# Kernel tuning notes

Hardware: AMD Instinct MI355X
Metric: run time of the kernel (lower is better)

## Reference

```python
import jax, jax.numpy as jnp
import numpy as np

N, E = 50000, 800000
IN, H, D, K = 256, 4, 64, 3
NEG_SLOPE = 0.2

def leaky_relu(x):
    return jnp.where(x >= 0, x, NEG_SLOPE * x)

def setup_inputs() -> dict:
    key = jax.random.key(0)
    ks = jax.random.split(key, 10)
    feat = jax.random.normal(ks[0], (N, IN), dtype=jnp.float32)
    src = jax.random.randint(ks[1], (E,), 0, N)
    dst = jax.random.randint(ks[2], (E,), 0, N)
    g = np.sqrt(2.0)  # relu gain used by xavier init; scale irrelevant to math
    W_src = jax.random.normal(ks[3], (H * D, IN), dtype=jnp.float32) * (g * np.sqrt(2.0 / (IN + H * D)))
    attn_l = jax.random.normal(ks[4], (1, H, D), dtype=jnp.float32) * 0.1
    attn_r = jax.random.normal(ks[5], (1, H, D), dtype=jnp.float32) * 0.1
    hop_attn_l = jax.random.normal(ks[6], (1, H, D), dtype=jnp.float32) * 0.1
    hop_attn_r = jax.random.normal(ks[7], (1, H, D), dtype=jnp.float32) * 0.1
    pos_emb = jax.random.normal(ks[8], (1, H, K + 1, D), dtype=jnp.float32) * 0.1
    bias = jnp.zeros((H * D,), dtype=jnp.float32)
    return {"feat": feat, "src": src, "dst": dst, "W_src": W_src,
            "attn_l": attn_l, "attn_r": attn_r, "hop_attn_l": hop_attn_l,
            "hop_attn_r": hop_attn_r, "pos_emb": pos_emb, "bias": bias}

def edge_softmax_dst(e, dst):
    # e: [E, H], softmax over incoming edges of each dst node
    m = jax.ops.segment_max(e, dst, num_segments=N)          # [N, H]
    m = jnp.where(jnp.isfinite(m), m, 0.0)                   # empty segments
    ex = jnp.exp(e - m[dst])                                 # [E, H]
    s = jax.ops.segment_sum(ex, dst, num_segments=N)         # [N, H]
    denom = s[dst]
    return jnp.where(denom > 0, ex / denom, 0.0)

def reference(feat, src, dst, W_src, attn_l, attn_r, hop_attn_l, hop_attn_r, pos_emb, bias):
    # fc_src (shared with fc_dst): [N, IN] -> [N, H, D]
    feat_src = (feat @ W_src.T).reshape(N, H, D)
    feat_dst = feat_src  # share_weights=True
    # GAT transition matrix, norm_by='dst'
    el = jnp.sum(feat_src * attn_l, axis=-1)   # [N, H]
    er = jnp.sum(feat_dst * attn_r, axis=-1)   # [N, H]
    e = leaky_relu(el[src] + er[dst])          # [E, H]
    a = edge_softmax_dst(e, dst)               # [E, H]
    # K-hop diffusion with positional embedding per hop
    h = feat_src
    hstack = [h + pos_emb[:, :, 0, :]]
    for k in range(1, K + 1):
        msg = a[:, :, None] * h[src]                          # [E, H, D]
        h = jax.ops.segment_sum(msg, dst, num_segments=N)     # [N, H, D]
        hstack.append(h + pos_emb[:, :, k, :])
    hs = jnp.stack(hstack, axis=2)                            # [N, H, K+1, D]
    # Hop-wise attention (HA)
    a_l = jnp.sum(hs * hop_attn_l[:, :, None, :], axis=-1, keepdims=True)            # [N,H,K+1,1]
    a_r = jnp.sum(hs[:, :, :1, :] * hop_attn_r[:, :, None, :], axis=-1, keepdims=True)  # [N,H,1,1]
    hop_a = jax.nn.softmax(leaky_relu(a_l + a_r), axis=2)
    rst = jnp.sum(hs * hop_a, axis=2)                         # [N, H, D]
    rst = rst + bias.reshape(1, H, D)
    return rst
```

## Files before the change

kernel.cpp:

```cpp
#include <hip/hip_runtime.h>
#include <hip/hip_bf16.h>
#include <hip/hip_fp16.h>

#define NN 50000
#define EE 800000
#define INF_ 256
#define HH 4
#define DD 64
#define KK 3
#define NEG_SLOPE 0.2f

struct __align__(8) half4 { __half2 a, b; };
struct __align__(8) short4s { short a, b, c, d; };

using bf16x8 = __attribute__((ext_vector_type(8))) short;
using f32x4  = __attribute__((ext_vector_type(4))) float;

__device__ __forceinline__ float lrelu(float x) {
    return x >= 0.0f ? x : NEG_SLOPE * x;
}

__device__ __forceinline__ float wave_sum(float v) {
    #pragma unroll
    for (int m = 1; m < 64; m <<= 1) v += __shfl_xor(v, m, 64);
    return v;
}

__device__ __forceinline__ short f2bf(float f) {
    union { float f; unsigned u; } v; v.f = f;
    unsigned r = (v.u + 0x7FFFu + ((v.u >> 16) & 1u)) >> 16;
    return (short)r;
}
__device__ __forceinline__ float bf2f(short s) {
    union { unsigned u; float f; } v; v.u = ((unsigned)(unsigned short)s) << 16;
    return v.f;
}

__global__ __launch_bounds__(256) void conv_w(const float* __restrict__ W,
                                              short* __restrict__ Wh,
                                              short* __restrict__ Wl) {
    int i = blockIdx.x * 256 + threadIdx.x;
    int e    = i & 7;
    int lane = (i >> 3) & 63;
    int tj   = (i >> 9) & 3;
    int kc   = (i >> 11) & 7;
    int w    = i >> 14;
    int j = w * 64 + tj * 16 + (lane & 15);
    int k = kc * 32 + (lane >> 4) * 8 + e;
    float v = W[j * 256 + k];
    short h = f2bf(v);
    Wh[i] = h;
    Wl[i] = f2bf(v - bf2f(h));
}

__global__ __launch_bounds__(256) void gemm_mfma(const float* __restrict__ A,
                                                 const short* __restrict__ Wh,
                                                 const short* __restrict__ Wl,
                                                 const float* __restrict__ al,
                                                 const float* __restrict__ ar,
                                                 float* __restrict__ C,
                                                 __half* __restrict__ C16,
                                                 float* __restrict__ el,
                                                 float* __restrict__ er, int M) {
    __shared__ short Ah[32 * 256];
    __shared__ short Al[32 * 256];
    int tid = threadIdx.x;
    int m0 = blockIdx.x * 32;

    {
        int r4 = tid >> 6;
        int c4 = (tid & 63) * 4;
        #pragma unroll
        for (int it = 0; it < 8; ++it) {
            int row = it * 4 + r4;
            int m = m0 + row;
            float4 v = (m < M) ? *(const float4*)&A[(size_t)m * 256 + c4]
                               : make_float4(0.f, 0.f, 0.f, 0.f);
            short h0 = f2bf(v.x), h1 = f2bf(v.y), h2 = f2bf(v.z), h3 = f2bf(v.w);
            short l0 = f2bf(v.x - bf2f(h0)), l1 = f2bf(v.y - bf2f(h1));
            short l2 = f2bf(v.z - bf2f(h2)), l3 = f2bf(v.w - bf2f(h3));
            int cs = c4 ^ ((row & 7) << 3);
            short4s sh = { h0, h1, h2, h3 };
            short4s sl = { l0, l1, l2, l3 };
            *(short4s*)&Ah[row * 256 + cs] = sh;
            *(short4s*)&Al[row * 256 + cs] = sl;
        }
    }
    __syncthreads();

    int w = tid >> 6;
    int lane = tid & 63;
    int lrow = lane & 15;
    int lk = lane >> 4;
    int j0 = w * 64;

    f32x4 acc[2][4] = {};

    #pragma unroll
    for (int kc = 0; kc < 8; ++kc) {
        int kbase = kc * 32 + lk * 8;
        int fbase = (((w * 8 + kc) * 4) * 64 + lane) * 8;
        bf16x8 bh[4], bl[4], ah[2], alo[2];
        #pragma unroll
        for (int tj = 0; tj < 4; ++tj) {
            bh[tj] = *(const bf16x8*)&Wh[fbase + tj * 64 * 8];
            bl[tj] = *(const bf16x8*)&Wl[fbase + tj * 64 * 8];
        }
        #pragma unroll
        for (int tm = 0; tm < 2; ++tm) {
            int row = tm * 16 + lrow;
            int ks = kbase ^ ((row & 7) << 3);
            ah[tm]  = *(const bf16x8*)&Ah[row * 256 + ks];
            alo[tm] = *(const bf16x8*)&Al[row * 256 + ks];
        }
        #pragma unroll
        for (int tm = 0; tm < 2; ++tm)
            #pragma unroll
            for (int tj = 0; tj < 4; ++tj) {
                acc[tm][tj] = __builtin_amdgcn_mfma_f32_16x16x32_bf16(ah[tm],  bh[tj], acc[tm][tj], 0, 0, 0);
                acc[tm][tj] = __builtin_amdgcn_mfma_f32_16x16x32_bf16(alo[tm], bh[tj], acc[tm][tj], 0, 0, 0);
                acc[tm][tj] = __builtin_amdgcn_mfma_f32_16x16x32_bf16(ah[tm],  bl[tj], acc[tm][tj], 0, 0, 0);
            }
    }

    #pragma unroll
    for (int tm = 0; tm < 2; ++tm)
        #pragma unroll
        for (int tj = 0; tj < 4; ++tj)
            #pragma unroll
            for (int r = 0; r < 4; ++r) {
                int m = m0 + tm * 16 + lk * 4 + r;
                if (m < M) {
                    int j = j0 + tj * 16 + lrow;
                    float x = acc[tm][tj][r];
                    C[(size_t)m * 256 + j] = x;
                    C16[(size_t)m * 256 + j] = __float2half(x);
                }
            }

    float alj[4], arj[4];
    #pragma unroll
    for (int tj = 0; tj < 4; ++tj) {
        alj[tj] = al[j0 + tj * 16 + lrow];
        arj[tj] = ar[j0 + tj * 16 + lrow];
    }
    #pragma unroll
    for (int tm = 0; tm < 2; ++tm)
        #pragma unroll
        for (int r = 0; r < 4; ++r) {
            float pl = acc[tm][0][r] * alj[0] + acc[tm][1][r] * alj[1] +
                       acc[tm][2][r] * alj[2] + acc[tm][3][r] * alj[3];
            float pr = acc[tm][0][r] * arj[0] + acc[tm][1][r] * arj[1] +
                       acc[tm][2][r] * arj[2] + acc[tm][3][r] * arj[3];
            #pragma unroll
            for (int msk = 1; msk < 16; msk <<= 1) {
                pl += __shfl_xor(pl, msk, 64);
                pr += __shfl_xor(pr, msk, 64);
            }
            if (lrow == 0) {
                int m = m0 + tm * 16 + lk * 4 + r;
                if (m < M) { el[m * 4 + w] = pl; er[m * 4 + w] = pr; }
            }
        }
}

__global__ void count_k(const int* __restrict__ dst, int* __restrict__ cnt, int E) {
    int e = blockIdx.x * 256 + threadIdx.x;
    if (e < E) atomicAdd(&cnt[dst[e]], 1);
}

__global__ __launch_bounds__(256) void scan1(const int* __restrict__ counts,
                                             int* __restrict__ offs,
                                             int* __restrict__ bsums, int n) {
    __shared__ int sh[256];
    int b = blockIdx.x, t = threadIdx.x;
    int base = b * 1024 + t * 4;
    int v[4];
    #pragma unroll
    for (int i = 0; i < 4; ++i) v[i] = (base + i < n) ? counts[base + i] : 0;
    int tsum = v[0] + v[1] + v[2] + v[3];
    sh[t] = tsum; __syncthreads();
    for (int off = 1; off < 256; off <<= 1) {
        int x = (t >= off) ? sh[t - off] : 0;
        __syncthreads();
        sh[t] += x;
        __syncthreads();
    }
    int run = sh[t] - tsum;
    #pragma unroll
    for (int i = 0; i < 4; ++i) { if (base + i < n) offs[base + i] = run; run += v[i]; }
    if (t == 255) bsums[b] = sh[255];
}

__global__ void scan2(int* bsums, int nb) {
    if (threadIdx.x == 0 && blockIdx.x == 0) {
        int run = 0;
        for (int i = 0; i < nb; ++i) { int v = bsums[i]; bsums[i] = run; run += v; }
    }
}

__global__ __launch_bounds__(256) void scan3(int* __restrict__ offs,
                                             const int* __restrict__ bsums,
                                             int* __restrict__ cursor, int n, int E) {
    int b = blockIdx.x;
    int base = b * 1024 + threadIdx.x * 4;
    int add = bsums[b];
    #pragma unroll
    for (int i = 0; i < 4; ++i) {
        if (base + i < n) {
            int v = offs[base + i] + add;
            offs[base + i] = v;
            cursor[base + i] = v;
        }
    }
    if (b == 0 && threadIdx.x == 0) offs[n] = E;
}

__global__ void scatter_edges(const int* __restrict__ src, const int* __restrict__ dst,
                              const float4* __restrict__ el4, const float4* __restrict__ er4,
                              int* __restrict__ cursor, int* __restrict__ ssrc,
                              float4* __restrict__ alog, int E) {
    int e = blockIdx.x * 256 + threadIdx.x;
    if (e >= E) return;
    int s = src[e], d = dst[e];
    int slot = atomicAdd(&cursor[d], 1);
    ssrc[slot] = s;
    float4 a = el4[s], b = er4[d];
    float4 o;
    o.x = lrelu(a.x + b.x);
    o.y = lrelu(a.y + b.y);
    o.z = lrelu(a.z + b.z);
    o.w = lrelu(a.w + b.w);
    alog[slot] = o;
}

__global__ __launch_bounds__(256) void edge_softmax(const int* __restrict__ offs,
                                                    float* __restrict__ alog, int n) {
    int t = blockIdx.x * 256 + threadIdx.x;
    if (t >= n * 4) return;
    int node = t >> 2, h = t & 3;
    int o0 = offs[node], o1 = offs[node + 1];
    if (o0 >= o1) return;
    float m = -1e30f;
    for (int i = o0; i < o1; ++i) m = fmaxf(m, alog[i * 4 + h]);
    float s = 0.f;
    for (int i = o0; i < o1; ++i) {
        float v = expf(alog[i * 4 + h] - m);
        alog[i * 4 + h] = v;
        s += v;
    }
    float inv = 1.0f / s;
    for (int i = o0; i < o1; ++i) alog[i * 4 + h] *= inv;
}

__global__ __launch_bounds__(256) void hop_kernel(const int* __restrict__ offs,
                                                  const int* __restrict__ ssrc,
                                                  const float* __restrict__ alog,
                                                  const __half* __restrict__ hin,
                                                  __half* __restrict__ hout) {
    int w = threadIdx.x >> 6;
    int n = blockIdx.x * 4 + w;
    if (n >= NN) return;
    int lane = threadIdx.x & 63;
    int h = lane >> 4;
    int col = lane * 4;
    int o0 = offs[n], o1 = offs[n + 1];
    float4 acc0 = make_float4(0.f, 0.f, 0.f, 0.f);
    float4 acc1 = make_float4(0.f, 0.f, 0.f, 0.f);
    float4 acc2 = make_float4(0.f, 0.f, 0.f, 0.f);
    float4 acc3 = make_float4(0.f, 0.f, 0.f, 0.f);
    int i = o0;
    for (; i + 4 <= o1; i += 4) {
        int s0 = ssrc[i], s1 = ssrc[i + 1], s2 = ssrc[i + 2], s3 = ssrc[i + 3];
        float a0 = alog[i * 4 + h];
        float a1 = alog[(i + 1) * 4 + h];
        float a2 = alog[(i + 2) * 4 + h];
        float a3 = alog[(i + 3) * 4 + h];
        half4 v0 = *(const half4*)&hin[(size_t)s0 * 256 + col];
        half4 v1 = *(const half4*)&hin[(size_t)s1 * 256 + col];
        half4 v2 = *(const half4*)&hin[(size_t)s2 * 256 + col];
        half4 v3 = *(const half4*)&hin[(size_t)s3 * 256 + col];
        float2 f0a = __half22float2(v0.a), f0b = __half22float2(v0.b);
        float2 f1a = __half22float2(v1.a), f1b = __half22float2(v1.b);
        float2 f2a = __half22float2(v2.a), f2b = __half22float2(v2.b);
        float2 f3a = __half22float2(v3.a), f3b = __half22float2(v3.b);
        acc0.x = fmaf(a0, f0a.x, acc0.x); acc0.y = fmaf(a0, f0a.y, acc0.y);
        acc0.z = fmaf(a0, f0b.x, acc0.z); acc0.w = fmaf(a0, f0b.y, acc0.w);
        acc1.x = fmaf(a1, f1a.x, acc1.x); acc1.y = fmaf(a1, f1a.y, acc1.y);
        acc1.z = fmaf(a1, f1b.x, acc1.z); acc1.w = fmaf(a1, f1b.y, acc1.w);
        acc2.x = fmaf(a2, f2a.x, acc2.x); acc2.y = fmaf(a2, f2a.y, acc2.y);
        acc2.z = fmaf(a2, f2b.x, acc2.z); acc2.w = fmaf(a2, f2b.y, acc2.w);
        acc3.x = fmaf(a3, f3a.x, acc3.x); acc3.y = fmaf(a3, f3a.y, acc3.y);
        acc3.z = fmaf(a3, f3b.x, acc3.z); acc3.w = fmaf(a3, f3b.y, acc3.w);
    }
    for (; i < o1; ++i) {
        int s0 = ssrc[i];
        float a0 = alog[i * 4 + h];
        half4 v0 = *(const half4*)&hin[(size_t)s0 * 256 + col];
        float2 f0a = __half22float2(v0.a), f0b = __half22float2(v0.b);
        acc0.x = fmaf(a0, f0a.x, acc0.x); acc0.y = fmaf(a0, f0a.y, acc0.y);
        acc0.z = fmaf(a0, f0b.x, acc0.z); acc0.w = fmaf(a0, f0b.y, acc0.w);
    }
    float4 r;
    r.x = (acc0.x + acc1.x) + (acc2.x + acc3.x);
    r.y = (acc0.y + acc1.y) + (acc2.y + acc3.y);
    r.z = (acc0.z + acc1.z) + (acc2.z + acc3.z);
    r.w = (acc0.w + acc1.w) + (acc2.w + acc3.w);
    half4 q;
    q.a = __floats2half2_rn(r.x, r.y);
    q.b = __floats2half2_rn(r.z, r.w);
    *(half4*)&hout[(size_t)n * 256 + col] = q;
}

__global__ __launch_bounds__(256) void hop_attn(const float* __restrict__ h0,
                                                const __half* __restrict__ h1,
                                                const __half* __restrict__ h2,
                                                const __half* __restrict__ h3,
                                                const float* __restrict__ pos,
                                                const float* __restrict__ hl,
                                                const float* __restrict__ hr,
                                                const float* __restrict__ bias,
                                                float* __restrict__ out) {
    int n = blockIdx.x, tid = threadIdx.x;
    int h = tid >> 6, d = tid & 63;
    size_t idx = (size_t)n * 256 + tid;
    float v0 = h0[idx] + pos[(h * 4 + 0) * 64 + d];
    float v1 = __half2float(h1[idx]) + pos[(h * 4 + 1) * 64 + d];
    float v2 = __half2float(h2[idx]) + pos[(h * 4 + 2) * 64 + d];
    float v3 = __half2float(h3[idx]) + pos[(h * 4 + 3) * 64 + d];
    float wl = hl[tid], wr = hr[tid];
    float r0 = wave_sum(v0 * wl);
    float r1 = wave_sum(v1 * wl);
    float r2 = wave_sum(v2 * wl);
    float r3 = wave_sum(v3 * wl);
    float ar = wave_sum(v0 * wr);
    float l0 = lrelu(r0 + ar), l1 = lrelu(r1 + ar), l2 = lrelu(r2 + ar), l3 = lrelu(r3 + ar);
    float mm = fmaxf(fmaxf(l0, l1), fmaxf(l2, l3));
    float e0 = expf(l0 - mm), e1 = expf(l1 - mm), e2 = expf(l2 - mm), e3 = expf(l3 - mm);
    float inv = 1.0f / (e0 + e1 + e2 + e3);
    out[idx] = (v0 * e0 + v1 * e1 + v2 * e2 + v3 * e3) * inv + bias[tid];
}

extern "C" void kernel_launch(void* const* d_in, const int* in_sizes, int n_in,
                              void* d_out, int out_size, void* d_ws, size_t ws_size,
                              hipStream_t stream) {
    const float* feat   = (const float*)d_in[0];
    const int*   src    = (const int*)d_in[1];
    const int*   dst    = (const int*)d_in[2];
    const float* W_src  = (const float*)d_in[3];
    const float* attn_l = (const float*)d_in[4];
    const float* attn_r = (const float*)d_in[5];
    const float* hop_l  = (const float*)d_in[6];
    const float* hop_r  = (const float*)d_in[7];
    const float* pos    = (const float*)d_in[8];
    const float* bias   = (const float*)d_in[9];
    float* out = (float*)d_out;

    char* p = (char*)d_ws;
    auto alloc = [&](size_t bytes) {
        char* r = p;
        p += (bytes + 255) & ~(size_t)255;
        return r;
    };
    float*  fs   = (float*)alloc((size_t)NN * 256 * 4);
    __half* fs16 = (__half*)alloc((size_t)NN * 256 * 2);
    __half* h1   = (__half*)alloc((size_t)NN * 256 * 2);
    __half* h2   = (__half*)alloc((size_t)NN * 256 * 2);
    __half* h3   = (__half*)alloc((size_t)NN * 256 * 2);
    int*   offs = (int*)alloc((size_t)(NN + 1) * 4);
    int*   cnt  = (int*)alloc((size_t)NN * 4);
    int*   cur  = (int*)alloc((size_t)NN * 4);
    int*   bsum = (int*)alloc(256);
    float* el   = (float*)alloc((size_t)NN * 4 * 4);
    float* er   = (float*)alloc((size_t)NN * 4 * 4);
    int*   ssrc = (int*)alloc((size_t)EE * 4);
    float* alog = (float*)alloc((size_t)EE * 4 * 4);
    short* Wh   = (short*)alloc((size_t)256 * 256 * 2);
    short* Wl   = (short*)alloc((size_t)256 * 256 * 2);

    const int nScan = (NN + 1023) / 1024;

    conv_w<<<256, 256, 0, stream>>>(W_src, Wh, Wl);
    gemm_mfma<<<(NN + 31) / 32, 256, 0, stream>>>(feat, Wh, Wl, attn_l, attn_r,
                                                  fs, fs16, el, er, NN);
    hipMemsetAsync(cnt, 0, (size_t)NN * 4, stream);
    count_k<<<(EE + 255) / 256, 256, 0, stream>>>(dst, cnt, EE);
    scan1<<<nScan, 256, 0, stream>>>(cnt, offs, bsum, NN);
    scan2<<<1, 64, 0, stream>>>(bsum, nScan);
    scan3<<<nScan, 256, 0, stream>>>(offs, bsum, cur, NN, EE);
    scatter_edges<<<(EE + 255) / 256, 256, 0, stream>>>(src, dst, (const float4*)el,
                                                        (const float4*)er, cur, ssrc,
                                                        (float4*)alog, EE);
    edge_softmax<<<(NN * 4 + 255) / 256, 256, 0, stream>>>(offs, alog, NN);
    hop_kernel<<<(NN + 3) / 4, 256, 0, stream>>>(offs, ssrc, alog, fs16, h1);
    hop_kernel<<<(NN + 3) / 4, 256, 0, stream>>>(offs, ssrc, alog, h1, h2);
    hop_kernel<<<(NN + 3) / 4, 256, 0, stream>>>(offs, ssrc, alog, h2, h3);
    hop_attn<<<NN, 256, 0, stream>>>(fs, h1, h2, h3, pos, hop_l, hop_r, bias, out);
}
```

Baseline: 515.2 us.

## Precompute hop-attention logits in producer kernels, simplify final combine

Hop-attention dot products are now computed where each hop's features are produced: in the GEMM epilogue for hop 0 and in each hop_kernel epilogue for hops 1-3. Positional-embedding contributions are handled by a tiny constants kernel, and a separate kernel computes the per-node hop softmax weights. The final hop_attn kernel then does only a weighted sum, with no wave reductions or exponentials. This removes five 64-lane reductions per thread from the final pass, at the cost of two extra launches, small extra buffers, and slightly different rounding because the logits use unrounded fp32 values rather than fp16-rounded hop features.

```diff
diff --git a/kernel.cpp b/kernel.cpp
--- a/kernel.cpp
+++ b/kernel.cpp
@@ -53,15 +53,33 @@
     Wl[i] = f2bf(v - bf2f(h));
 }
 
+__global__ void pconsts(const float* __restrict__ pos, const float* __restrict__ hl,
+                        const float* __restrict__ hr, float* __restrict__ pC,
+                        float* __restrict__ pR) {
+    int d = threadIdx.x;
+    for (int h = 0; h < 4; ++h) {
+        float vr = wave_sum(pos[(h * 4 + 0) * 64 + d] * hr[h * 64 + d]);
+        if (d == 0) pR[h] = vr;
+        for (int k = 0; k < 4; ++k) {
+            float vl = wave_sum(pos[(h * 4 + k) * 64 + d] * hl[h * 64 + d]);
+            if (d == 0) pC[h * 4 + k] = vl;
+        }
+    }
+}
+
 __global__ __launch_bounds__(256) void gemm_mfma(const float* __restrict__ A,
                                                  const short* __restrict__ Wh,
                                                  const short* __restrict__ Wl,
                                                  const float* __restrict__ al,
                                                  const float* __restrict__ ar,
+                                                 const float* __restrict__ hl,
+                                                 const float* __restrict__ hr,
                                                  float* __restrict__ C,
                                                  __half* __restrict__ C16,
                                                  float* __restrict__ el,
-                                                 float* __restrict__ er, int M) {
+                                                 float* __restrict__ er,
+                                                 float* __restrict__ hdl0,
+                                                 float* __restrict__ hdr0, int M) {
     __shared__ short Ah[32 * 256];
     __shared__ short Al[32 * 256];
     int tid = threadIdx.x;
@@ -138,11 +156,12 @@
                 }
             }
 
-    float alj[4], arj[4];
+    float alj[4], arj[4], hlj[4], hrj[4];
     #pragma unroll
     for (int tj = 0; tj < 4; ++tj) {
-        alj[tj] = al[j0 + tj * 16 + lrow];
-        arj[tj] = ar[j0 + tj * 16 + lrow];
+        int j = j0 + tj * 16 + lrow;
+        alj[tj] = al[j]; arj[tj] = ar[j];
+        hlj[tj] = hl[j]; hrj[tj] = hr[j];
     }
     #pragma unroll
     for (int tm = 0; tm < 2; ++tm)
@@ -152,14 +171,23 @@
                        acc[tm][2][r] * alj[2] + acc[tm][3][r] * alj[3];
             float pr = acc[tm][0][r] * arj[0] + acc[tm][1][r] * arj[1] +
                        acc[tm][2][r] * arj[2] + acc[tm][3][r] * arj[3];
+            float ph = acc[tm][0][r] * hlj[0] + acc[tm][1][r] * hlj[1] +
+                       acc[tm][2][r] * hlj[2] + acc[tm][3][r] * hlj[3];
+            float pq = acc[tm][0][r] * hrj[0] + acc[tm][1][r] * hrj[1] +
+                       acc[tm][2][r] * hrj[2] + acc[tm][3][r] * hrj[3];
             #pragma unroll
             for (int msk = 1; msk < 16; msk <<= 1) {
                 pl += __shfl_xor(pl, msk, 64);
                 pr += __shfl_xor(pr, msk, 64);
+                ph += __shfl_xor(ph, msk, 64);
+                pq += __shfl_xor(pq, msk, 64);
             }
             if (lrow == 0) {
                 int m = m0 + tm * 16 + lk * 4 + r;
-                if (m < M) { el[m * 4 + w] = pl; er[m * 4 + w] = pr; }
+                if (m < M) {
+                    el[m * 4 + w] = pl;  er[m * 4 + w] = pr;
+                    hdl0[m * 4 + w] = ph; hdr0[m * 4 + w] = pq;
+                }
             }
         }
 }
@@ -257,7 +285,9 @@
                                                   const int* __restrict__ ssrc,
                                                   const float* __restrict__ alog,
                                                   const __half* __restrict__ hin,
-                                                  __half* __restrict__ hout) {
+                                                  __half* __restrict__ hout,
+                                                  const float* __restrict__ hl,
+                                                  float* __restrict__ hdl) {
     int w = threadIdx.x >> 6;
     int n = blockIdx.x * 4 + w;
     if (n >= NN) return;
@@ -310,6 +340,32 @@
     q.a = __floats2half2_rn(r.x, r.y);
     q.b = __floats2half2_rn(r.z, r.w);
     *(half4*)&hout[(size_t)n * 256 + col] = q;
+    float pd = r.x * hl[col] + r.y * hl[col + 1] + r.z * hl[col + 2] + r.w * hl[col + 3];
+    #pragma unroll
+    for (int msk = 1; msk < 16; msk <<= 1) pd += __shfl_xor(pd, msk, 64);
+    if ((lane & 15) == 0) hdl[n * 4 + h] = pd;
+}
+
+__global__ __launch_bounds__(256) void hop_wts(const float* __restrict__ hdl0,
+                                               const float* __restrict__ hdl1,
+                                               const float* __restrict__ hdl2,
+                                               const float* __restrict__ hdl3,
+                                               const float* __restrict__ hdr0,
+                                               const float* __restrict__ pC,
+                                               const float* __restrict__ pR,
+                                               float4* __restrict__ wts, int n4) {
+    int t = blockIdx.x * 256 + threadIdx.x;
+    if (t >= n4) return;
+    int h = t & 3;
+    float ar = hdr0[t] + pR[h];
+    float l0 = lrelu(hdl0[t] + pC[h * 4 + 0] + ar);
+    float l1 = lrelu(hdl1[t] + pC[h * 4 + 1] + ar);
+    float l2 = lrelu(hdl2[t] + pC[h * 4 + 2] + ar);
+    float l3 = lrelu(hdl3[t] + pC[h * 4 + 3] + ar);
+    float mm = fmaxf(fmaxf(l0, l1), fmaxf(l2, l3));
+    float e0 = expf(l0 - mm), e1 = expf(l1 - mm), e2 = expf(l2 - mm), e3 = expf(l3 - mm);
+    float inv = 1.0f / (e0 + e1 + e2 + e3);
+    wts[t] = make_float4(e0 * inv, e1 * inv, e2 * inv, e3 * inv);
 }
 
 __global__ __launch_bounds__(256) void hop_attn(const float* __restrict__ h0,
@@ -317,28 +373,18 @@
                                                 const __half* __restrict__ h2,
                                                 const __half* __restrict__ h3,
                                                 const float* __restrict__ pos,
-                                                const float* __restrict__ hl,
-                                                const float* __restrict__ hr,
+                                                const float4* __restrict__ wts,
                                                 const float* __restrict__ bias,
                                                 float* __restrict__ out) {
     int n = blockIdx.x, tid = threadIdx.x;
     int h = tid >> 6, d = tid & 63;
     size_t idx = (size_t)n * 256 + tid;
+    float4 w = wts[n * 4 + h];
     float v0 = h0[idx] + pos[(h * 4 + 0) * 64 + d];
     float v1 = __half2float(h1[idx]) + pos[(h * 4 + 1) * 64 + d];
     float v2 = __half2float(h2[idx]) + pos[(h * 4 + 2) * 64 + d];
     float v3 = __half2float(h3[idx]) + pos[(h * 4 + 3) * 64 + d];
-    float wl = hl[tid], wr = hr[tid];
-    float r0 = wave_sum(v0 * wl);
-    float r1 = wave_sum(v1 * wl);
-    float r2 = wave_sum(v2 * wl);
-    float r3 = wave_sum(v3 * wl);
-    float ar = wave_sum(v0 * wr);
-    float l0 = lrelu(r0 + ar), l1 = lrelu(r1 + ar), l2 = lrelu(r2 + ar), l3 = lrelu(r3 + ar);
-    float mm = fmaxf(fmaxf(l0, l1), fmaxf(l2, l3));
-    float e0 = expf(l0 - mm), e1 = expf(l1 - mm), e2 = expf(l2 - mm), e3 = expf(l3 - mm);
-    float inv = 1.0f / (e0 + e1 + e2 + e3);
-    out[idx] = (v0 * e0 + v1 * e1 + v2 * e2 + v3 * e3) * inv + bias[tid];
+    out[idx] = v0 * w.x + v1 * w.y + v2 * w.z + v3 * w.w + bias[tid];
 }
 
 extern "C" void kernel_launch(void* const* d_in, const int* in_sizes, int n_in,
@@ -377,12 +423,22 @@
     float* alog = (float*)alloc((size_t)EE * 4 * 4);
     short* Wh   = (short*)alloc((size_t)256 * 256 * 2);
     short* Wl   = (short*)alloc((size_t)256 * 256 * 2);
+    float* hdl0 = (float*)alloc((size_t)NN * 4 * 4);
+    float* hdr0 = (float*)alloc((size_t)NN * 4 * 4);
+    float* hdl1 = (float*)alloc((size_t)NN * 4 * 4);
+    float* hdl2 = (float*)alloc((size_t)NN * 4 * 4);
+    float* hdl3 = (float*)alloc((size_t)NN * 4 * 4);
+    float* wts  = (float*)alloc((size_t)NN * 4 * 16);
+    float* pC   = (float*)alloc(16 * 4);
+    float* pR   = (float*)alloc(4 * 4);
 
     const int nScan = (NN + 1023) / 1024;
 
     conv_w<<<256, 256, 0, stream>>>(W_src, Wh, Wl);
+    pconsts<<<1, 64, 0, stream>>>(pos, hop_l, hop_r, pC, pR);
     gemm_mfma<<<(NN + 31) / 32, 256, 0, stream>>>(feat, Wh, Wl, attn_l, attn_r,
-                                                  fs, fs16, el, er, NN);
+                                                  hop_l, hop_r, fs, fs16, el, er,
+                                                  hdl0, hdr0, NN);
     hipMemsetAsync(cnt, 0, (size_t)NN * 4, stream);
     count_k<<<(EE + 255) / 256, 256, 0, stream>>>(dst, cnt, EE);
     scan1<<<nScan, 256, 0, stream>>>(cnt, offs, bsum, NN);
@@ -392,8 +448,10 @@
                                                         (const float4*)er, cur, ssrc,
                                                         (float4*)alog, EE);
     edge_softmax<<<(NN * 4 + 255) / 256, 256, 0, stream>>>(offs, alog, NN);
-    hop_kernel<<<(NN + 3) / 4, 256, 0, stream>>>(offs, ssrc, alog, fs16, h1);
-    hop_kernel<<<(NN + 3) / 4, 256, 0, stream>>>(offs, ssrc, alog, h1, h2);
-    hop_kernel<<<(NN + 3) / 4, 256, 0, stream>>>(offs, ssrc, alog, h2, h3);
-    hop_attn<<<NN, 256, 0, stream>>>(fs, h1, h2, h3, pos, hop_l, hop_r, bias, out);
-}
+    hop_kernel<<<(NN + 3) / 4, 256, 0, stream>>>(offs, ssrc, alog, fs16, h1, hop_l, hdl1);
+    hop_kernel<<<(NN + 3) / 4, 256, 0, stream>>>(offs, ssrc, alog, h1, h2, hop_l, hdl2);
+    hop_kernel<<<(NN + 3) / 4, 256, 0, stream>>>(offs, ssrc, alog, h2, h3, hop_l, hdl3);
+    hop_wts<<<(NN * 4 + 255) / 256, 256, 0, stream>>>(hdl0, hdl1, hdl2, hdl3, hdr0,
+                                                      pC, pR, (float4*)wts, NN * 4);
+    hop_attn<<<NN, 256, 0, stream>>>(fs, h1, h2, h3, pos, (const float4*)wts, bias, out);
+}
```

Result: faster. 492.8 us (-4.3%).
